# Optimization experiments

Hardware: AMD Instinct MI355X
Metric: run time of the kernel (lower is better)

## Reference

```python
import jax, jax.numpy as jnp
import numpy as np
import math

D_MODEL = 512
NUM_HEADS = 8
D_HEAD = D_MODEL // NUM_HEADS
B, S = 4, 2048
L = 2 * S - 1  # relative position range


def _rel_shift(pos_score):
    # pos_score: [B, H, S, L] -> [B, H, S, L//2+1] via pad/reshape/slice trick
    b, h, s, l = pos_score.shape
    padded = jnp.pad(pos_score, ((0, 0), (0, 0), (0, 0), (1, 0)))  # [B,H,S,L+1]
    padded = padded.reshape(b, h, l + 1, s)
    shifted = padded[:, :, 1:].reshape(b, h, s, l)
    return shifted[..., : l // 2 + 1]


def setup_inputs() -> dict:
    key = jax.random.key(0)
    ks = jax.random.split(key, 16)
    std = 1.0 / math.sqrt(D_MODEL)
    inp = {
        "query": jax.random.normal(ks[0], (B, S, D_MODEL), jnp.float32),
        "key": jax.random.normal(ks[1], (B, S, D_MODEL), jnp.float32),
        "value": jax.random.normal(ks[2], (B, S, D_MODEL), jnp.float32),
        "pos_embedding": jax.random.normal(ks[3], (B, L, D_MODEL), jnp.float32),
        "Wq": jax.random.normal(ks[4], (D_MODEL, D_MODEL), jnp.float32) * std,
        "bq": jnp.zeros((D_MODEL,), jnp.float32),
        "Wk": jax.random.normal(ks[5], (D_MODEL, D_MODEL), jnp.float32) * std,
        "bk": jnp.zeros((D_MODEL,), jnp.float32),
        "Wv": jax.random.normal(ks[6], (D_MODEL, D_MODEL), jnp.float32) * std,
        "bv": jnp.zeros((D_MODEL,), jnp.float32),
        "Wp": jax.random.normal(ks[7], (D_MODEL, D_MODEL), jnp.float32) * std,
        "u_bias": jax.random.normal(ks[8], (NUM_HEADS, D_HEAD), jnp.float32) * std,
        "v_bias": jax.random.normal(ks[9], (NUM_HEADS, D_HEAD), jnp.float32) * std,
        "Wo": jax.random.normal(ks[10], (D_MODEL, D_MODEL), jnp.float32) * std,
        "bo": jnp.zeros((D_MODEL,), jnp.float32),
    }
    return inp


def reference(query, key, value, pos_embedding, Wq, bq, Wk, bk, Wv, bv, Wp, u_bias, v_bias, Wo, bo):
    b, s, d = query.shape
    h, dh = u_bias.shape
    sqrt_dim = jnp.asarray(math.sqrt(d), query.dtype)

    q = (query @ Wq.T + bq).reshape(b, s, h, dh)
    k = (key @ Wk.T + bk).reshape(b, -1, h, dh)
    v = (value @ Wv.T + bv).reshape(b, -1, h, dh)
    p = (pos_embedding @ Wp.T).reshape(b, -1, h, dh)

    content_score = jnp.einsum("bshd,bthd->bhst", q + u_bias, k)
    pos_score = jnp.einsum("bshd,blhd->bhsl", q + v_bias, p)
    pos_score = _rel_shift(pos_score)  # [B,H,S,S]

    score = (content_score + pos_score) / sqrt_dim
    attn = jax.nn.softmax(score, axis=-1)
    context = jnp.einsum("bhst,bthd->bshd", attn, v).reshape(b, s, d)
    return context @ Wo.T + bo
```

## Files before the change

### kernel.cpp

```cpp
#include <hip/hip_runtime.h>


typedef __bf16 bf16;
typedef __bf16 bf16x4 __attribute__((ext_vector_type(4)));
typedef __bf16 bf16x8 __attribute__((ext_vector_type(8)));
typedef float  f32x4  __attribute__((ext_vector_type(4)));

#define MFMA(A,B,C) __builtin_amdgcn_mfma_f32_16x16x32_bf16((A),(B),(C),0,0,0)

constexpr float SCP = 1.44269504088896f / 22.6274169979695f;

__device__ __forceinline__ void gload16(const void* g, void* l) {
    __builtin_amdgcn_global_load_lds(
        (const __attribute__((address_space(1))) void*)g,
        (__attribute__((address_space(3))) void*)l, 16, 0, 0);
}

constexpr size_t WBYTES   = 512u*512u*2u;
constexpr size_t OFF_WQ   = 0;
constexpr size_t OFF_WK   = OFF_WQ + WBYTES;
constexpr size_t OFF_WV   = OFF_WK + WBYTES;
constexpr size_t OFF_WP   = OFF_WV + WBYTES;
constexpr size_t OFF_WO   = OFF_WP + WBYTES;
constexpr size_t QKV_BYTES = 4ull*8*2048*64*2;
constexpr size_t OFF_QU   = OFF_WO + WBYTES;
constexpr size_t OFF_QV   = OFF_QU + QKV_BYTES;
constexpr size_t OFF_KK   = OFF_QV + QKV_BYTES;
constexpr size_t OFF_VT   = OFF_KK + QKV_BYTES;
constexpr size_t OFF_PP   = OFF_VT + QKV_BYTES;
constexpr size_t PP_BYTES = 4ull*8*4096*64*2;
constexpr size_t OFF_CTX  = OFF_PP + PP_BYTES;

__global__ __launch_bounds__(256) void convert_weights(
    const float* __restrict__ w0, const float* __restrict__ w1,
    const float* __restrict__ w2, const float* __restrict__ w3,
    const float* __restrict__ w4, bf16* __restrict__ dst)
{
    int idx = blockIdx.x * 256 + threadIdx.x;
    const float* srcs[5] = {w0, w1, w2, w3, w4};
    int which = idx >> 15;
    int off   = (idx & 32767) * 8;
    const float* s = srcs[which] + off;
    float4 a = *(const float4*)s;
    float4 b = *(const float4*)(s + 4);
    bf16x8 o;
    o[0]=(bf16)a.x; o[1]=(bf16)a.y; o[2]=(bf16)a.z; o[3]=(bf16)a.w;
    o[4]=(bf16)b.x; o[5]=(bf16)b.y; o[6]=(bf16)b.z; o[7]=(bf16)b.w;
    *(bf16x8*)(dst + (size_t)which * (512*512) + off) = o;
}

template<int MODE>
__global__ __launch_bounds__(256) void gemm_k(
    const void* __restrict__ Av, const bf16* __restrict__ Bw,
    const float* __restrict__ bias, const float* __restrict__ ub,
    const float* __restrict__ vb,
    bf16* __restrict__ o0, bf16* __restrict__ o1, float* __restrict__ of, int M)
{
    __shared__ __align__(16) bf16 As[128 * 64];
    const int tid = threadIdx.x, lane = tid & 63, w = tid >> 6;
    const int r = lane & 15, g = lane >> 4;
    const int m0 = blockIdx.x * 128, n0 = blockIdx.y * 128;
    const int wr = (w >> 1) * 64, wc = (w & 1) * 64;
    f32x4 acc[4][4] = {};

    for (int kt = 0; kt < 512; kt += 64) {
        __syncthreads();
        #pragma unroll
        for (int i = 0; i < 4; i++) {
            int gi = tid + 256 * i;
            int row = gi >> 3, c8 = gi & 7;
            int gm = m0 + row;
            bf16x8 v8;
            if constexpr (MODE == 4) {
                v8 = *(const bf16x8*)((const bf16*)Av + (size_t)gm * 512 + kt + c8 * 8);
            } else {
                float4 a0 = {0,0,0,0}, a1 = {0,0,0,0};
                if (MODE != 3 || gm < M) {
                    const float* ap = (const float*)Av + (size_t)gm * 512 + kt + c8 * 8;
                    a0 = *(const float4*)ap;
                    a1 = *(const float4*)(ap + 4);
                }
                v8[0]=(bf16)a0.x; v8[1]=(bf16)a0.y; v8[2]=(bf16)a0.z; v8[3]=(bf16)a0.w;
                v8[4]=(bf16)a1.x; v8[5]=(bf16)a1.y; v8[6]=(bf16)a1.z; v8[7]=(bf16)a1.w;
            }
            *(bf16x8*)((char*)As + row * 128 + ((c8 ^ (row & 7)) << 4)) = v8;
        }
        __syncthreads();
        #pragma unroll
        for (int ks = 0; ks < 2; ks++) {
            bf16x8 af[4], bfr[4];
            #pragma unroll
            for (int rt = 0; rt < 4; rt++) {
                int row = wr + rt * 16 + r;
                af[rt] = *(const bf16x8*)((const char*)As + row * 128 +
                                          (((ks * 4 + g) ^ (row & 7)) << 4));
            }
            #pragma unroll
            for (int ct = 0; ct < 4; ct++) {
                int n = n0 + wc + ct * 16 + r;
                bfr[ct] = *(const bf16x8*)(Bw + (size_t)n * 512 + kt + ks * 32 + g * 8);
            }
            #pragma unroll
            for (int rt = 0; rt < 4; rt++)
                #pragma unroll
                for (int ct = 0; ct < 4; ct++)
                    acc[rt][ct] = MFMA(af[rt], bfr[ct], acc[rt][ct]);
        }
    }

    #pragma unroll
    for (int rt = 0; rt < 4; rt++) {
        #pragma unroll
        for (int ct = 0; ct < 4; ct++) {
            int gn = n0 + wc + ct * 16 + r;
            int rb = m0 + wr + rt * 16 + g * 4;
            float bsum = (MODE == 3) ? 0.f : bias[gn];
            #pragma unroll
            for (int i = 0; i < 4; i++) {
                int gm = rb + i;
                float val = acc[rt][ct][i];
                if constexpr (MODE == 0) {
                    int b = gm >> 11, s = gm & 2047, h = gn >> 6, dh = gn & 63;
                    size_t o = ((size_t)((b * 8 + h) * 2048 + s)) * 64 + dh;
                    float qb = val + bsum;
                    o0[o] = (bf16)((qb + ub[gn]) * SCP);
                    o1[o] = (bf16)((qb + vb[gn]) * SCP);
                } else if constexpr (MODE == 1) {
                    int b = gm >> 11, s = gm & 2047, h = gn >> 6, dh = gn & 63;
                    o0[((size_t)((b * 8 + h) * 2048 + s)) * 64 +
                       (dh ^ ((s & 7) << 3))] = (bf16)(val + bsum);
                } else if constexpr (MODE == 2) {
                    int b = gm >> 11, s = gm & 2047, h = gn >> 6, dh = gn & 63;
                    int sc = s & 63, sb = s & ~63;
                    o0[((size_t)((b * 8 + h) * 64 + dh)) * 2048 + sb +
                       (sc ^ ((dh & 7) << 3))] = (bf16)(val + bsum);
                } else if constexpr (MODE == 3) {
                    if (gm < M) {
                        int b = gm / 4095, l = gm - b * 4095, h = gn >> 6, dh = gn & 63;
                        o0[((size_t)((b * 8 + h) * 4096 + l)) * 64 + dh] = (bf16)val;
                    }
                } else {
                    of[(size_t)gm * 512 + gn] = val + bsum;
                }
            }
        }
    }
}

__global__ __launch_bounds__(512, 4) void attn_k(
    const bf16* __restrict__ qu, const bf16* __restrict__ qv,
    const bf16* __restrict__ kk, const bf16* __restrict__ vt,
    const bf16* __restrict__ pp, bf16* __restrict__ ctx)
{
    __shared__ __align__(16) bf16 kls[2][64 * 64];
    __shared__ __align__(16) bf16 vls[2][64 * 64];
    __shared__ __align__(16) bf16 ps2[128][84];
    __shared__ __align__(16) bf16 at_t[128 * 64];

    const int lane = threadIdx.x & 63, w = threadIdx.x >> 6;
    const int r = lane & 15, g = lane >> 4;
    const int sw = (r & 7) << 4;
    const int bid = blockIdx.x;
    const int lbid = (bid & 7) * 64 + (bid >> 3);
    const int bh = lbid >> 4;
    const int sigma = lbid & 15;
    const int s0 = sigma << 7;

    const bf16* quB = qu + (size_t)bh * 2048 * 64;
    const bf16* qvB = qv + (size_t)bh * 2048 * 64;
    const bf16* kkB = kk + (size_t)bh * 2048 * 64;
    const bf16* vtB = vt + (size_t)bh * 64 * 2048;
    const bf16* ppB = pp + (size_t)bh * 4096 * 64;

    bf16x8 qaf0, qaf1, qvf0, qvf1;
    {
        const int srow = s0 + 16 * w + r;
        qaf0 = *(const bf16x8*)(quB + (size_t)srow * 64 + g * 8);
        qaf1 = *(const bf16x8*)(quB + (size_t)srow * 64 + 32 + g * 8);
        qvf0 = *(const bf16x8*)(qvB + (size_t)srow * 64 + g * 8);
        qvf1 = *(const bf16x8*)(qvB + (size_t)srow * 64 + 32 + g * 8);
    }
    __builtin_amdgcn_sched_barrier(0);

    bf16* psR = &ps2[16 * w + r][0];
    const int lq = lane >> 3, lc = (lane & 7) << 4;

    bf16x8 pfP[10];
    {
        const int tp = ((sigma * 2) & 31) << 6;
        gload16((const char*)kkB + ((size_t)(tp + w * 8 + lq) << 7) + lc,
                (char*)kls[0] + w * 1024);
        gload16((const char*)vtB + ((size_t)(w * 8 + lq) << 12) + tp * 2 + lc,
                (char*)vls[0] + w * 1024);
        __builtin_amdgcn_sched_barrier(0);
        const int lbw = tp - s0 + 2032 - 16 * w;
        #pragma unroll
        for (int j = 0; j < 5; j++) {
            const bf16* pr = ppB + (size_t)(lbw + j * 16 + r) * 64 + g * 8;
            pfP[2*j]   = *(const bf16x8*)pr;
            pfP[2*j+1] = *(const bf16x8*)(pr + 32);
        }
        __builtin_amdgcn_sched_barrier(0);
    }

    f32x4 oacc[4] = {};
    float sum = 0.f;

    #pragma unroll 2
    for (int n = 0; n < 32; ++n) {
        const int cur = n & 1;
        asm volatile("s_waitcnt vmcnt(10)" ::: "memory");
        __builtin_amdgcn_s_barrier();
        __builtin_amdgcn_sched_barrier(0);

        {
            const int tn = ((sigma * 2 + n + 1) & 31) << 6;
            gload16((const char*)kkB + ((size_t)(tn + w * 8 + lq) << 7) + lc,
                    (char*)kls[cur ^ 1] + w * 1024);
            gload16((const char*)vtB + ((size_t)(w * 8 + lq) << 12) + tn * 2 + lc,
                    (char*)vls[cur ^ 1] + w * 1024);
        }
        __builtin_amdgcn_sched_barrier(0);

        #pragma unroll
        for (int j = 0; j < 5; j++) {
            f32x4 ps = {};
            ps = MFMA(pfP[2*j],   qvf0, ps);
            ps = MFMA(pfP[2*j+1], qvf1, ps);
            bf16x4 pb;
            pb[0]=(bf16)ps[0]; pb[1]=(bf16)ps[1]; pb[2]=(bf16)ps[2]; pb[3]=(bf16)ps[3];
            *(bf16x4*)(psR + j * 16 + g * 4) = pb;
        }

        f32x4 cc[4];
        #pragma unroll
        for (int c = 0; c < 4; c++) {
            const char* kb = (const char*)kls[cur] + (c * 16 + r) * 128;
            bf16x8 k0 = *(const bf16x8*)(kb + (( 0 + g * 16) ^ sw));
            bf16x8 k1 = *(const bf16x8*)(kb + ((64 + g * 16) ^ sw));
            f32x4 a = {};
            a = MFMA(k0, qaf0, a);
            a = MFMA(k1, qaf1, a);
            cc[c] = a;
        }

        {
            const int tn  = ((sigma * 2 + n + 1) & 31) << 6;
            const int lbw = tn - s0 + 2032 - 16 * w;
            #pragma unroll
            for (int j = 0; j < 5; j++) {
                const bf16* pr = ppB + (size_t)(lbw + j * 16 + r) * 64 + g * 8;
                pfP[2*j]   = *(const bf16x8*)pr;
                pfP[2*j+1] = *(const bf16x8*)(pr + 32);
            }
        }

        #pragma unroll
        for (int c = 0; c < 4; c++) {
            const int base = c * 16 + g * 4 + 15 - r;
            float p0 = psR[base], p1 = psR[base+1], p2 = psR[base+2], p3 = psR[base+3];
            float e0 = exp2f(cc[c][0] + p0);
            float e1 = exp2f(cc[c][1] + p1);
            float e2 = exp2f(cc[c][2] + p2);
            float e3 = exp2f(cc[c][3] + p3);
            sum += (e0 + e1) + (e2 + e3);
            bf16x4 pk;
            pk[0]=(bf16)e0; pk[1]=(bf16)e1; pk[2]=(bf16)e2; pk[3]=(bf16)e3;
            *(bf16x4*)((char*)at_t + (16 * w + r) * 128 + ((c * 32 + g * 8) ^ sw)) = pk;
        }

        #pragma unroll
        for (int ks = 0; ks < 2; ks++) {
            bf16x8 af = *(const bf16x8*)((const char*)at_t + (16 * w + r) * 128 +
                                         ((ks * 64 + g * 16) ^ sw));
            #pragma unroll
            for (int nt = 0; nt < 4; nt++) {
                const char* vb_ = (const char*)vls[cur] + (nt * 16 + r) * 128;
                bf16x8 vf = *(const bf16x8*)(vb_ + ((ks * 64 + g * 16) ^ sw));
                oacc[nt] = MFMA(af, vf, oacc[nt]);
            }
        }
    }

    asm volatile("s_waitcnt vmcnt(0)" ::: "memory");

    sum += __shfl_xor(sum, 16);
    sum += __shfl_xor(sum, 32);
    const float inv = 1.f / sum;

    const int b = bh >> 3, h = bh & 7;
    #pragma unroll
    for (int nt = 0; nt < 4; nt++) {
        #pragma unroll
        for (int i = 0; i < 4; i++) {
            const float si = __shfl(inv, g * 4 + i);
            const int s = s0 + 16 * w + g * 4 + i;
            const int col = h * 64 + nt * 16 + r;
            ctx[((size_t)(b * 2048 + s)) * 512 + col] = (bf16)(oacc[nt][i] * si);
        }
    }
}

extern "C" void kernel_launch(void* const* d_in, const int* in_sizes, int n_in,
                              void* d_out, int out_size, void* d_ws, size_t ws_size,
                              hipStream_t stream)
{
    (void)in_sizes; (void)n_in; (void)out_size; (void)ws_size;
    const float* query = (const float*)d_in[0];
    const float* key_  = (const float*)d_in[1];
    const float* value = (const float*)d_in[2];
    const float* pos   = (const float*)d_in[3];
    const float* Wq = (const float*)d_in[4];  const float* bq = (const float*)d_in[5];
    const float* Wk = (const float*)d_in[6];  const float* bk = (const float*)d_in[7];
    const float* Wv = (const float*)d_in[8];  const float* bv = (const float*)d_in[9];
    const float* Wp = (const float*)d_in[10];
    const float* ub = (const float*)d_in[11]; const float* vb = (const float*)d_in[12];
    const float* Wo = (const float*)d_in[13]; const float* bo = (const float*)d_in[14];

    char* ws = (char*)d_ws;
    bf16* Wqb = (bf16*)(ws + OFF_WQ);
    bf16* Wkb = (bf16*)(ws + OFF_WK);
    bf16* Wvb = (bf16*)(ws + OFF_WV);
    bf16* Wpb = (bf16*)(ws + OFF_WP);
    bf16* Wob = (bf16*)(ws + OFF_WO);
    bf16* quP = (bf16*)(ws + OFF_QU);
    bf16* qvP = (bf16*)(ws + OFF_QV);
    bf16* kkP = (bf16*)(ws + OFF_KK);
    bf16* vtP = (bf16*)(ws + OFF_VT);
    bf16* ppP = (bf16*)(ws + OFF_PP);
    bf16* ctxP = (bf16*)(ws + OFF_CTX);

    convert_weights<<<640, 256, 0, stream>>>(Wq, Wk, Wv, Wp, Wo, (bf16*)(ws + OFF_WQ));

    gemm_k<0><<<dim3(64, 4), 256, 0, stream>>>(query, Wqb, bq, ub, vb, quP, qvP, nullptr, 8192);
    gemm_k<1><<<dim3(64, 4), 256, 0, stream>>>(key_,  Wkb, bk, nullptr, nullptr, kkP, nullptr, nullptr, 8192);
    gemm_k<2><<<dim3(64, 4), 256, 0, stream>>>(value, Wvb, bv, nullptr, nullptr, vtP, nullptr, nullptr, 8192);
    gemm_k<3><<<dim3(128, 4), 256, 0, stream>>>(pos,  Wpb, nullptr, nullptr, nullptr, ppP, nullptr, nullptr, 16380);

    attn_k<<<dim3(512), 512, 0, stream>>>(quP, qvP, kkP, vtP, ppP, ctxP);

    gemm_k<4><<<dim3(64, 4), 256, 0, stream>>>(ctxP, Wob, bo, nullptr, nullptr, nullptr, nullptr, (float*)d_out, 8192);
}
```

Measured before the change: 296.2 us.

## Merge projection GEMMs into one launch and load V fragments directly from global

Replaces the four separate projection GEMM launches with one 3D-grid kernel that chooses its input, weights and epilogue from blockIdx.z; blocks outside the Q/K/V row range return early. In the attention kernel, the V tile is no longer staged through LDS with async loads. Each wave instead reads its V MFMA operands straight from global memory in two halves, and the V transpose layout drops its XOR swizzle. This cuts launch overhead and LDS traffic, at the cost of more uncoalesced global loads, possible exposed latency in the inner loop, and runtime mode branches in the epilogue.

Result: slower. 446.6 us (+50.8%).

```diff
diff --git a/kernel.cpp b/kernel.cpp
--- a/kernel.cpp
+++ b/kernel.cpp
@@ -49,12 +49,107 @@
     *(bf16x8*)(dst + (size_t)which * (512*512) + off) = o;
 }
 
-template<int MODE>
-__global__ __launch_bounds__(256) void gemm_k(
-    const void* __restrict__ Av, const bf16* __restrict__ Bw,
-    const float* __restrict__ bias, const float* __restrict__ ub,
-    const float* __restrict__ vb,
-    bf16* __restrict__ o0, bf16* __restrict__ o1, float* __restrict__ of, int M)
+__global__ __launch_bounds__(256) void gemm_proj(
+    const float* __restrict__ Aq, const float* __restrict__ Ak,
+    const float* __restrict__ Av, const float* __restrict__ Ap,
+    const bf16* __restrict__ Wqb, const bf16* __restrict__ Wkb,
+    const bf16* __restrict__ Wvb, const bf16* __restrict__ Wpb,
+    const float* __restrict__ bq, const float* __restrict__ bk,
+    const float* __restrict__ bv,
+    const float* __restrict__ ub, const float* __restrict__ vb,
+    bf16* __restrict__ qu, bf16* __restrict__ qv, bf16* __restrict__ kk,
+    bf16* __restrict__ vt, bf16* __restrict__ pp)
+{
+    const int mode = blockIdx.z;
+    if (mode < 3 && blockIdx.x >= 64) return;
+    const float* A  = (mode == 0) ? Aq  : (mode == 1) ? Ak  : (mode == 2) ? Av  : Ap;
+    const bf16*  Bw = (mode == 0) ? Wqb : (mode == 1) ? Wkb : (mode == 2) ? Wvb : Wpb;
+
+    __shared__ __align__(16) bf16 As[128 * 64];
+    const int tid = threadIdx.x, lane = tid & 63, w = tid >> 6;
+    const int r = lane & 15, g = lane >> 4;
+    const int m0 = blockIdx.x * 128, n0 = blockIdx.y * 128;
+    const int wr = (w >> 1) * 64, wc = (w & 1) * 64;
+    f32x4 acc[4][4] = {};
+
+    for (int kt = 0; kt < 512; kt += 64) {
+        __syncthreads();
+        #pragma unroll
+        for (int i = 0; i < 4; i++) {
+            int gi = tid + 256 * i;
+            int row = gi >> 3, c8 = gi & 7;
+            int gm = m0 + row;
+            float4 a0 = {0,0,0,0}, a1 = {0,0,0,0};
+            if (mode != 3 || gm < 16380) {
+                const float* ap = A + (size_t)gm * 512 + kt + c8 * 8;
+                a0 = *(const float4*)ap;
+                a1 = *(const float4*)(ap + 4);
+            }
+            bf16x8 v8;
+            v8[0]=(bf16)a0.x; v8[1]=(bf16)a0.y; v8[2]=(bf16)a0.z; v8[3]=(bf16)a0.w;
+            v8[4]=(bf16)a1.x; v8[5]=(bf16)a1.y; v8[6]=(bf16)a1.z; v8[7]=(bf16)a1.w;
+            *(bf16x8*)((char*)As + row * 128 + ((c8 ^ (row & 7)) << 4)) = v8;
+        }
+        __syncthreads();
+        #pragma unroll
+        for (int ks = 0; ks < 2; ks++) {
+            bf16x8 af[4], bfr[4];
+            #pragma unroll
+            for (int rt = 0; rt < 4; rt++) {
+                int row = wr + rt * 16 + r;
+                af[rt] = *(const bf16x8*)((const char*)As + row * 128 +
+                                          (((ks * 4 + g) ^ (row & 7)) << 4));
+            }
+            #pragma unroll
+            for (int ct = 0; ct < 4; ct++) {
+                int n = n0 + wc + ct * 16 + r;
+                bfr[ct] = *(const bf16x8*)(Bw + (size_t)n * 512 + kt + ks * 32 + g * 8);
+            }
+            #pragma unroll
+            for (int rt = 0; rt < 4; rt++)
+                #pragma unroll
+                for (int ct = 0; ct < 4; ct++)
+                    acc[rt][ct] = MFMA(af[rt], bfr[ct], acc[rt][ct]);
+        }
+    }
+
+    #pragma unroll
+    for (int rt = 0; rt < 4; rt++) {
+        #pragma unroll
+        for (int ct = 0; ct < 4; ct++) {
+            int gn = n0 + wc + ct * 16 + r;
+            int rb = m0 + wr + rt * 16 + g * 4;
+            #pragma unroll
+            for (int i = 0; i < 4; i++) {
+                int gm = rb + i;
+                float val = acc[rt][ct][i];
+                if (mode == 0) {
+                    int b = gm >> 11, s = gm & 2047, h = gn >> 6, dh = gn & 63;
+                    size_t o = ((size_t)((b * 8 + h) * 2048 + s)) * 64 + dh;
+                    float qb = val + bq[gn];
+                    qu[o] = (bf16)((qb + ub[gn]) * SCP);
+                    qv[o] = (bf16)((qb + vb[gn]) * SCP);
+                } else if (mode == 1) {
+                    int b = gm >> 11, s = gm & 2047, h = gn >> 6, dh = gn & 63;
+                    kk[((size_t)((b * 8 + h) * 2048 + s)) * 64 +
+                       (dh ^ ((s & 7) << 3))] = (bf16)(val + bk[gn]);
+                } else if (mode == 2) {
+                    int b = gm >> 11, s = gm & 2047, h = gn >> 6, dh = gn & 63;
+                    vt[((size_t)((b * 8 + h) * 64 + dh)) * 2048 + s] = (bf16)(val + bv[gn]);
+                } else {
+                    if (gm < 16380) {
+                        int b = gm / 4095, l = gm - b * 4095, h = gn >> 6, dh = gn & 63;
+                        pp[((size_t)((b * 8 + h) * 4096 + l)) * 64 + dh] = (bf16)val;
+                    }
+                }
+            }
+        }
+    }
+}
+
+__global__ __launch_bounds__(256) void gemm_out(
+    const bf16* __restrict__ Ac, const bf16* __restrict__ Bw,
+    const float* __restrict__ bias, float* __restrict__ of)
 {
     __shared__ __align__(16) bf16 As[128 * 64];
     const int tid = threadIdx.x, lane = tid & 63, w = tid >> 6;
@@ -69,20 +164,7 @@
         for (int i = 0; i < 4; i++) {
             int gi = tid + 256 * i;
             int row = gi >> 3, c8 = gi & 7;
-            int gm = m0 + row;
-            bf16x8 v8;
-            if constexpr (MODE == 4) {
-                v8 = *(const bf16x8*)((const bf16*)Av + (size_t)gm * 512 + kt + c8 * 8);
-            } else {
-                float4 a0 = {0,0,0,0}, a1 = {0,0,0,0};
-                if (MODE != 3 || gm < M) {
-                    const float* ap = (const float*)Av + (size_t)gm * 512 + kt + c8 * 8;
-                    a0 = *(const float4*)ap;
-                    a1 = *(const float4*)(ap + 4);
-                }
-                v8[0]=(bf16)a0.x; v8[1]=(bf16)a0.y; v8[2]=(bf16)a0.z; v8[3]=(bf16)a0.w;
-                v8[4]=(bf16)a1.x; v8[5]=(bf16)a1.y; v8[6]=(bf16)a1.z; v8[7]=(bf16)a1.w;
-            }
+            bf16x8 v8 = *(const bf16x8*)(Ac + (size_t)(m0 + row) * 512 + kt + c8 * 8);
             *(bf16x8*)((char*)As + row * 128 + ((c8 ^ (row & 7)) << 4)) = v8;
         }
         __syncthreads();
@@ -107,44 +189,16 @@
                     acc[rt][ct] = MFMA(af[rt], bfr[ct], acc[rt][ct]);
         }
     }
-
     #pragma unroll
-    for (int rt = 0; rt < 4; rt++) {
+    for (int rt = 0; rt < 4; rt++)
         #pragma unroll
         for (int ct = 0; ct < 4; ct++) {
             int gn = n0 + wc + ct * 16 + r;
             int rb = m0 + wr + rt * 16 + g * 4;
-            float bsum = (MODE == 3) ? 0.f : bias[gn];
-            #pragma unroll
-            for (int i = 0; i < 4; i++) {
-                int gm = rb + i;
-                float val = acc[rt][ct][i];
-                if constexpr (MODE == 0) {
-                    int b = gm >> 11, s = gm & 2047, h = gn >> 6, dh = gn & 63;
-                    size_t o = ((size_t)((b * 8 + h) * 2048 + s)) * 64 + dh;
-                    float qb = val + bsum;
-                    o0[o] = (bf16)((qb + ub[gn]) * SCP);
-                    o1[o] = (bf16)((qb + vb[gn]) * SCP);
-                } else if constexpr (MODE == 1) {
-                    int b = gm >> 11, s = gm & 2047, h = gn >> 6, dh = gn & 63;
-                    o0[((size_t)((b * 8 + h) * 2048 + s)) * 64 +
-                       (dh ^ ((s & 7) << 3))] = (bf16)(val + bsum);
-                } else if constexpr (MODE == 2) {
-                    int b = gm >> 11, s = gm & 2047, h = gn >> 6, dh = gn & 63;
-                    int sc = s & 63, sb = s & ~63;
-                    o0[((size_t)((b * 8 + h) * 64 + dh)) * 2048 + sb +
-                       (sc ^ ((dh & 7) << 3))] = (bf16)(val + bsum);
-                } else if constexpr (MODE == 3) {
-                    if (gm < M) {
-                        int b = gm / 4095, l = gm - b * 4095, h = gn >> 6, dh = gn & 63;
-                        o0[((size_t)((b * 8 + h) * 4096 + l)) * 64 + dh] = (bf16)val;
-                    }
-                } else {
-                    of[(size_t)gm * 512 + gn] = val + bsum;
-                }
-            }
-        }
-    }
+            #pragma unroll
+            for (int i = 0; i < 4; i++)
+                of[(size_t)(rb + i) * 512 + gn] = acc[rt][ct][i] + bias[gn];
+        }
 }
 
 __global__ __launch_bounds__(512, 4) void attn_k(
@@ -153,7 +207,6 @@
     const bf16* __restrict__ pp, bf16* __restrict__ ctx)
 {
     __shared__ __align__(16) bf16 kls[2][64 * 64];
-    __shared__ __align__(16) bf16 vls[2][64 * 64];
     __shared__ __align__(16) bf16 ps2[128][84];
     __shared__ __align__(16) bf16 at_t[128 * 64];
 
@@ -190,8 +243,6 @@
         const int tp = ((sigma * 2) & 31) << 6;
         gload16((const char*)kkB + ((size_t)(tp + w * 8 + lq) << 7) + lc,
                 (char*)kls[0] + w * 1024);
-        gload16((const char*)vtB + ((size_t)(w * 8 + lq) << 12) + tp * 2 + lc,
-                (char*)vls[0] + w * 1024);
         __builtin_amdgcn_sched_barrier(0);
         const int lbw = tp - s0 + 2032 - 16 * w;
         #pragma unroll
@@ -208,17 +259,20 @@
 
     #pragma unroll 2
     for (int n = 0; n < 32; ++n) {
+        const int t0 = ((sigma * 2 + n) & 31) << 6;
         const int cur = n & 1;
         asm volatile("s_waitcnt vmcnt(10)" ::: "memory");
         __builtin_amdgcn_s_barrier();
         __builtin_amdgcn_sched_barrier(0);
 
+        bf16x8 vf0[4];
+        #pragma unroll
+        for (int nt = 0; nt < 4; nt++)
+            vf0[nt] = *(const bf16x8*)(vtB + (size_t)(nt * 16 + r) * 2048 + t0 + g * 8);
         {
             const int tn = ((sigma * 2 + n + 1) & 31) << 6;
             gload16((const char*)kkB + ((size_t)(tn + w * 8 + lq) << 7) + lc,
                     (char*)kls[cur ^ 1] + w * 1024);
-            gload16((const char*)vtB + ((size_t)(w * 8 + lq) << 12) + tn * 2 + lc,
-                    (char*)vls[cur ^ 1] + w * 1024);
         }
         __builtin_amdgcn_sched_barrier(0);
 
@@ -250,10 +304,14 @@
             #pragma unroll
             for (int j = 0; j < 5; j++) {
                 const bf16* pr = ppB + (size_t)(lbw + j * 16 + r) * 64 + g * 8;
-                pfP[2*j]   = *(const bf16x8*)pr;
+                pfP[2*j]   = *(const bf16x8*)(pr);
                 pfP[2*j+1] = *(const bf16x8*)(pr + 32);
             }
         }
+        bf16x8 vf1[4];
+        #pragma unroll
+        for (int nt = 0; nt < 4; nt++)
+            vf1[nt] = *(const bf16x8*)(vtB + (size_t)(nt * 16 + r) * 2048 + t0 + 32 + g * 8);
 
         #pragma unroll
         for (int c = 0; c < 4; c++) {
@@ -269,16 +327,17 @@
             *(bf16x4*)((char*)at_t + (16 * w + r) * 128 + ((c * 32 + g * 8) ^ sw)) = pk;
         }
 
-        #pragma unroll
-        for (int ks = 0; ks < 2; ks++) {
-            bf16x8 af = *(const bf16x8*)((const char*)at_t + (16 * w + r) * 128 +
-                                         ((ks * 64 + g * 16) ^ sw));
-            #pragma unroll
-            for (int nt = 0; nt < 4; nt++) {
-                const char* vb_ = (const char*)vls[cur] + (nt * 16 + r) * 128;
-                bf16x8 vf = *(const bf16x8*)(vb_ + ((ks * 64 + g * 16) ^ sw));
-                oacc[nt] = MFMA(af, vf, oacc[nt]);
-            }
+        {
+            bf16x8 af0 = *(const bf16x8*)((const char*)at_t + (16 * w + r) * 128 +
+                                          ((0 + g * 16) ^ sw));
+            #pragma unroll
+            for (int nt = 0; nt < 4; nt++)
+                oacc[nt] = MFMA(af0, vf0[nt], oacc[nt]);
+            bf16x8 af1 = *(const bf16x8*)((const char*)at_t + (16 * w + r) * 128 +
+                                          ((64 + g * 16) ^ sw));
+            #pragma unroll
+            for (int nt = 0; nt < 4; nt++)
+                oacc[nt] = MFMA(af1, vf1[nt], oacc[nt]);
         }
     }
 
@@ -332,12 +391,11 @@
 
     convert_weights<<<640, 256, 0, stream>>>(Wq, Wk, Wv, Wp, Wo, (bf16*)(ws + OFF_WQ));
 
-    gemm_k<0><<<dim3(64, 4), 256, 0, stream>>>(query, Wqb, bq, ub, vb, quP, qvP, nullptr, 8192);
-    gemm_k<1><<<dim3(64, 4), 256, 0, stream>>>(key_,  Wkb, bk, nullptr, nullptr, kkP, nullptr, nullptr, 8192);
-    gemm_k<2><<<dim3(64, 4), 256, 0, stream>>>(value, Wvb, bv, nullptr, nullptr, vtP, nullptr, nullptr, 8192);
-    gemm_k<3><<<dim3(128, 4), 256, 0, stream>>>(pos,  Wpb, nullptr, nullptr, nullptr, ppP, nullptr, nullptr, 16380);
+    gemm_proj<<<dim3(128, 4, 4), 256, 0, stream>>>(
+        query, key_, value, pos, Wqb, Wkb, Wvb, Wpb,
+        bq, bk, bv, ub, vb, quP, qvP, kkP, vtP, ppP);
 
     attn_k<<<dim3(512), 512, 0, stream>>>(quP, qvP, kkP, vtP, ppP, ctxP);
 
-    gemm_k<4><<<dim3(64, 4), 256, 0, stream>>>(ctxP, Wob, bo, nullptr, nullptr, nullptr, nullptr, (float*)d_out, 8192);
-}
+    gemm_out<<<dim3(64, 4), 256, 0, stream>>>(ctxP, Wob, bo, (float*)d_out);
+}
```
